# Performance work log

Measured on AMD Instinct MI355X. Metric: run time of the kernel, lower is better.

## Reference

```python
import jax, jax.numpy as jnp
import numpy as np

N_FM = 100000; N_TP = 4096; N_SM = 100000
IN_FM = 64; IN_SM = 32; IN_TP = 32; IN_GF = 64; HID = 128
E_QOQ = 1000000; E_BP = 1000000; E_CP = 500000; E_CD = 500000; E_RB = 1000000


def setup_inputs():
    key = jax.random.key(0)
    ks = jax.random.split(key, 32)
    rn = lambda k, s, sc=0.05: jax.random.normal(k, s, jnp.float32) * sc
    inp = {}
    inp['x_fm'] = jax.random.normal(ks[0], (N_FM, IN_FM), jnp.float32)
    inp['x_sm'] = jax.random.normal(ks[1], (N_SM, IN_SM), jnp.float32)
    inp['period_vol'] = jax.random.uniform(ks[2], (N_TP, 1), jnp.float32)
    inp['gf'] = jax.random.normal(ks[3], (1, IN_GF), jnp.float32)
    inp['pe_table'] = rn(ks[4], (N_TP, IN_TP), 1.0)  # period_emb weight
    inp['qoq_src'] = jax.random.randint(ks[5], (E_QOQ,), 0, N_FM)
    inp['qoq_dst'] = jax.random.randint(ks[6], (E_QOQ,), 0, N_FM)
    inp['bp_src'] = jax.random.randint(ks[7], (E_BP,), 0, N_FM)
    inp['bp_dst'] = jax.random.randint(ks[8], (E_BP,), 0, N_TP)
    inp['cp_src'] = jax.random.randint(ks[9], (E_CP,), 0, N_TP)
    inp['cp_dst'] = jax.random.randint(ks[10], (E_CP,), 0, N_FM)
    inp['cd_src'] = jax.random.randint(ks[11], (E_CD,), 0, N_TP)
    inp['cd_dst'] = jax.random.randint(ks[12], (E_CD,), 0, N_SM)
    inp['rb_src'] = jax.random.randint(ks[13], (E_RB,), 0, N_TP)
    inp['rb_dst'] = jax.random.randint(ks[14], (E_RB,), 0, N_FM)
    i = 15
    # per-relation SAGEConv params: W_l [in_src,H] + bias, W_r [in_dst,H] (root, no bias)
    for name, ins, ind in [('qoq', IN_FM, IN_FM), ('bp', IN_FM, IN_TP), ('cp', IN_TP, IN_FM), ('cd', IN_TP, IN_SM), ('rb', IN_TP, IN_FM)]:
        inp[name + '_Wl'] = rn(ks[i], (ins, HID)); inp[name + '_bl'] = jnp.zeros((HID,), jnp.float32)
        inp[name + '_Wr'] = rn(ks[i + 1], (ind, HID)); i += 2
    for t in ['fm', 'tp', 'sm']:
        inp['ln_' + t + '_g'] = jnp.ones((HID,), jnp.float32)
        inp['ln_' + t + '_b'] = jnp.zeros((HID,), jnp.float32)
    inp['head_W1'] = rn(ks[i], (HID * 3 + IN_GF, HID // 2)); inp['head_b1'] = jnp.zeros((HID // 2,), jnp.float32)
    inp['head_W2'] = rn(ks[i + 1], (HID // 2, 1)); inp['head_b2'] = jnp.zeros((1,), jnp.float32)
    return inp


def _seg_mean(feat, dst, n):
    s = jax.ops.segment_sum(feat, dst, num_segments=n)
    c = jax.ops.segment_sum(jnp.ones((dst.shape[0], 1), feat.dtype), dst, num_segments=n)
    return s / jnp.maximum(c, 1.0)


def _sage(x_src, x_dst, src, dst, Wl, bl, Wr):
    # PyG SAGEConv: lin_l(mean_j x_j) + lin_r(x_i); aggregate raw features, then transform
    m = _seg_mean(x_src[src], dst, x_dst.shape[0])
    return m @ Wl + bl + x_dst @ Wr


def _ln(x, g, b, eps=1e-5):
    mu = x.mean(-1, keepdims=True)
    xc = x - mu
    var = (xc * xc).mean(-1, keepdims=True)
    return xc / jnp.sqrt(var + eps) * g + b


def _forward(x_fm, x_sm, period_vol, gf, pe_table,
             qoq_Wl, qoq_bl, qoq_Wr, bp_Wl, bp_bl, bp_Wr, cp_Wl, cp_bl, cp_Wr,
             cd_Wl, cd_bl, cd_Wr, rb_Wl, rb_bl, rb_Wr,
             ln_fm_g, ln_fm_b, ln_tp_g, ln_tp_b, ln_sm_g, ln_sm_b,
             head_W1, head_b1, head_W2, head_b2,
             qoq_src, qoq_dst, bp_src, bp_dst, cp_src, cp_dst, cd_src, cd_dst, rb_src, rb_dst):
    pe = pe_table * period_vol  # [T, in_tp]
    # HeteroConv aggr='mean': average relation outputs per destination type
    out_fm = (_sage(x_fm, x_fm, qoq_src, qoq_dst, qoq_Wl, qoq_bl, qoq_Wr)
              + _sage(pe, x_fm, cp_src, cp_dst, cp_Wl, cp_bl, cp_Wr)
              + _sage(pe, x_fm, rb_src, rb_dst, rb_Wl, rb_bl, rb_Wr)) / 3.0
    out_tp = _sage(x_fm, pe, bp_src, bp_dst, bp_Wl, bp_bl, bp_Wr)
    out_sm = _sage(pe, x_sm, cd_src, cd_dst, cd_Wl, cd_bl, cd_Wr)
    fm = jax.nn.relu(_ln(out_fm, ln_fm_g, ln_fm_b))
    tp = jax.nn.relu(_ln(out_tp, ln_tp_g, ln_tp_b))
    sm = jax.nn.relu(_ln(out_sm, ln_sm_g, ln_sm_b))
    h = jnp.concatenate([fm.mean(0), tp.mean(0), sm.mean(0), gf[0]], axis=-1)
    h = jax.nn.relu(h @ head_W1 + head_b1)  # dropout is identity in eval
    return (h @ head_W2 + head_b2).squeeze()


def reference(x_fm, x_sm, period_vol, gf, pe_table,
              qoq_src, qoq_dst, bp_src, bp_dst, cp_src, cp_dst, cd_src, cd_dst, rb_src, rb_dst,
              qoq_Wl, qoq_bl, qoq_Wr, bp_Wl, bp_bl, bp_Wr, cp_Wl, cp_bl, cp_Wr,
              cd_Wl, cd_bl, cd_Wr, rb_Wl, rb_bl, rb_Wr,
              ln_fm_g, ln_fm_b, ln_tp_g, ln_tp_b, ln_sm_g, ln_sm_b,
              head_W1, head_b1, head_W2, head_b2):
    return _forward(x_fm, x_sm, period_vol, gf, pe_table,
                    qoq_Wl, qoq_bl, qoq_Wr, bp_Wl, bp_bl, bp_Wr, cp_Wl, cp_bl, cp_Wr,
                    cd_Wl, cd_bl, cd_Wr, rb_Wl, rb_bl, rb_Wr,
                    ln_fm_g, ln_fm_b, ln_tp_g, ln_tp_b, ln_sm_g, ln_sm_b,
                    head_W1, head_b1, head_W2, head_b2,
                    qoq_src, qoq_dst, bp_src, bp_dst, cp_src, cp_dst, cd_src, cd_dst, rb_src, rb_dst)
```

## Files before the change

### kernel.cpp

```cpp
#include <hip/hip_runtime.h>
#include <hip/hip_fp16.h>

#define N_FM 100000
#define N_TP 4096
#define N_SM 100000
#define HID 128
#define E_QOQ 1000000
#define E_BP 1000000
#define E_CP 500000
#define E_CD 500000
#define E_RB 1000000
#define E_TOT 4000000

#define EO_CP  1000000
#define EO_RB  1500000
#define EO_BP  2500000
#define EO_CD  3500000

#define EL_QOQ 0
#define EL_CP  (N_FM)
#define EL_RB  (2 * N_FM)
#define EL_BP  (3 * N_FM)
#define EL_CD  (3 * N_FM + N_TP)
#define NTOT   (3 * N_FM + N_TP + N_SM)

#define BB_QOQ 0
#define BB_CP  782
#define BB_RB  1173
#define BB_BP  1564
#define BB_CD  1692
#define NBUCK  2083
#define CHUNK  4096
#define NCHUNK ((E_TOT + CHUNK - 1) / CHUNK)
#define EPB    (CHUNK / 256)

#define PAIRS_CAP 5784064

#define GRID_FM 768
#define GRID_TP 64
#define GRID_SM 1024

__device__ __forceinline__ int bucket_base(int b) {
    if (b < BB_CP) return b * 2048;
    if (b < BB_RB) return 1601536 + (b - BB_CP) * 2048;
    if (b < BB_BP) return 2402304 + (b - BB_RB) * 3584;
    if (b < BB_CD) return 3803648 + (b - BB_BP) * 9216;
    return 4983296 + (b - BB_CD) * 2048;
}

typedef _Float16 h2 __attribute__((ext_vector_type(2)));
typedef _Float16 f16x8_t __attribute__((ext_vector_type(8)));
typedef float f32x4_t __attribute__((ext_vector_type(4)));

union U32H2 { unsigned u; h2 h; };
union U4H8 { uint4 u; f16x8_t h; };

#if defined(__has_builtin)
#if __has_builtin(__builtin_amdgcn_fdot2)
#define HAVE_FDOT2 1
#endif
#endif

__device__ __forceinline__ unsigned pk2(float a, float b) {
    U32H2 x; x.h = h2{(_Float16)a, (_Float16)b}; return x.u;
}
__device__ __forceinline__ f16x8_t as_h8(uint4 v) { U4H8 x; x.u = v; return x.h; }

__device__ __forceinline__ float dot2sel(float acc, h2 v, h2 sel) {
#ifdef HAVE_FDOT2
    return __builtin_amdgcn_fdot2(v, sel, acc, false);
#else
    return acc + (float)v[0] * (float)sel[0] + (float)v[1] * (float)sel[1];
#endif
}

#define R1 (N_FM * 32)
#define R2 (R1 + N_SM * 16)
#define R3 (R2 + N_TP * 16)
#define R4 (R3 + 12288)
#define R5 (R4 + 6144)
#define R6 (R5 + 4096)
#define R7 (R6 + 128)

__device__ __forceinline__ unsigned pack_pair(const float* W, int p, int c) {
    return pk2(W[(2 * p) * HID + c], W[(2 * p + 1) * HID + c]);
}

__global__ void pack_all(const float* __restrict__ x_fm, const float* __restrict__ x_sm,
                         const float* __restrict__ pe_table, const float* __restrict__ pvol,
                         const float* __restrict__ qoq_Wl, const float* __restrict__ cp_Wl,
                         const float* __restrict__ rb_Wl, const float* __restrict__ qoq_Wr,
                         const float* __restrict__ cp_Wr, const float* __restrict__ rb_Wr,
                         const float* __restrict__ bp_Wl, const float* __restrict__ bp_Wr,
                         const float* __restrict__ cd_Wl, const float* __restrict__ cd_Wr,
                         const float* __restrict__ qoq_bl, const float* __restrict__ cp_bl,
                         const float* __restrict__ rb_bl,
                         unsigned* __restrict__ x_fm_f, unsigned* __restrict__ x_sm_f,
                         unsigned* __restrict__ pe_f, unsigned* __restrict__ wf_fm,
                         unsigned* __restrict__ wf_tp, unsigned* __restrict__ wf_sm,
                         float* __restrict__ bias_fm) {
    int gid = blockIdx.x * blockDim.x + threadIdx.x;
    if (gid < R1) {
        float2 t = ((const float2*)x_fm)[gid];
        x_fm_f[gid] = pk2(t.x, t.y);
    } else if (gid < R2) {
        int i = gid - R1;
        float2 t = ((const float2*)x_sm)[i];
        x_sm_f[i] = pk2(t.x, t.y);
    } else if (gid < R3) {
        int i = gid - R2;
        float2 t = ((const float2*)pe_table)[i];
        float v = pvol[i >> 4];
        pe_f[i] = pk2(t.x * v, t.y * v);
    } else if (gid < R4) {
        int j = gid - R3;
        int f = j >> 8, lr = (j >> 2) & 63, jj = j & 3;
        int p = (f >> 3) * 16 + ((lr >> 4) << 2) + jj;
        int c = (f & 7) * 16 + (lr & 15);
        unsigned v;
        if (p < 32) v = pack_pair(qoq_Wl, p, c);
        else if (p < 48) v = pack_pair(cp_Wl, p - 32, c);
        else if (p < 64) v = pack_pair(rb_Wl, p - 48, c);
        else {
            int pp = p - 64;
            float u0 = qoq_Wr[(2 * pp) * HID + c] + cp_Wr[(2 * pp) * HID + c] + rb_Wr[(2 * pp) * HID + c];
            float u1 = qoq_Wr[(2 * pp + 1) * HID + c] + cp_Wr[(2 * pp + 1) * HID + c] + rb_Wr[(2 * pp + 1) * HID + c];
            v = pk2(u0, u1);
        }
        wf_fm[j] = v;
    } else if (gid < R5) {
        int j = gid - R4;
        int f = j >> 8, lr = (j >> 2) & 63, jj = j & 3;
        int p = (f >> 3) * 16 + ((lr >> 4) << 2) + jj;
        int c = (f & 7) * 16 + (lr & 15);
        wf_tp[j] = (p < 32) ? pack_pair(bp_Wl, p, c) : pack_pair(bp_Wr, p - 32, c);
    } else if (gid < R6) {
        int j = gid - R5;
        int f = j >> 8, lr = (j >> 2) & 63, jj = j & 3;
        int p = (f >> 3) * 16 + ((lr >> 4) << 2) + jj;
        int c = (f & 7) * 16 + (lr & 15);
        wf_sm[j] = (p < 16) ? pack_pair(cd_Wl, p, c) : pack_pair(cd_Wr, p - 16, c);
    } else if (gid < R7) {
        int c = gid - R6;
        bias_fm[c] = qoq_bl[c] + cp_bl[c] + rb_bl[c];
    }
}

struct EdgePtrs {
    const int *qs, *qd, *cs, *cd_, *rs, *rd, *bs, *bd, *ds, *dd;
};

template <bool NEED_SRC>
__device__ __forceinline__ void edge_decode(const EdgePtrs& P, int e, int& bucket, int& dl, int& src) {
    const int* dp = P.qd; const int* sp = P.qs;
    int i = e, bb = BB_QOQ, sh = 7;
    if (e >= EO_CP) { i = e - EO_CP; dp = P.cd_; sp = P.cs; bb = BB_CP; sh = 8; }
    if (e >= EO_RB) { i = e - EO_RB; dp = P.rd;  sp = P.rs; bb = BB_RB; sh = 8; }
    if (e >= EO_BP) { i = e - EO_BP; dp = P.bd;  sp = P.bs; bb = BB_BP; sh = 5; }
    if (e >= EO_CD) { i = e - EO_CD; dp = P.dd;  sp = P.ds; bb = BB_CD; sh = 8; }
    int d = dp[i];
    bucket = bb + (d >> sh);
    dl = d & ((1 << sh) - 1);
    if (NEED_SRC) src = sp[i];
}

__global__ void __launch_bounds__(256) bin_kernel(EdgePtrs P, int* __restrict__ bwork,
                                                  unsigned* __restrict__ pairs) {
    __shared__ int lh[NBUCK];
    const int tid = threadIdx.x;
    for (int i = tid; i < NBUCK; i += 256) lh[i] = 0;
    __syncthreads();
    const int base = blockIdx.x * CHUNK;
    const int lim = min(base + CHUNK, E_TOT);
    unsigned ebd[EPB]; int esr[EPB];
#pragma unroll
    for (int j = 0; j < EPB; j++) {
        int e = base + tid + j * 256;
        if (e < lim) {
            int b, dl, s;
            edge_decode<true>(P, e, b, dl, s);
            ebd[j] = ((unsigned)b << 8) | (unsigned)dl;
            esr[j] = s;
            atomicAdd(&lh[b], 1);
        }
    }
    __syncthreads();
#pragma unroll
    for (int u = 0; u < (NBUCK + 255) / 256; u++) {
        int b = tid + u * 256;
        if (b < NBUCK) {
            int c = lh[b];
            lh[b] = c ? bucket_base(b) + atomicAdd(&bwork[b], c) : 0;
        }
    }
    __syncthreads();
#pragma unroll
    for (int j = 0; j < EPB; j++) {
        int e = base + tid + j * 256;
        if (e < lim) {
            int b = (int)(ebd[j] >> 8);
            int pos = atomicAdd(&lh[b], 1);
            pairs[pos] = ((ebd[j] & 255u) << 24) | (unsigned)esr[j];
        }
    }
}

__global__ void __launch_bounds__(256) esort(const int* __restrict__ bwork,
                                             const unsigned* __restrict__ pairs,
                                             int* __restrict__ so,
                                             int* __restrict__ el_beg, int* __restrict__ el_end) {
    __shared__ int hist[256], scn[256];
    __shared__ int so_lds[9216];
    const int b = blockIdx.x;
    const int tid = threadIdx.x;
    int beg = bucket_base(b);
    int end = beg + bwork[b];
    int egbase, ne;
    if (b < BB_CP)      { int e0 = (b - BB_QOQ) << 7; egbase = EL_QOQ + e0; ne = min(128, N_FM - e0); }
    else if (b < BB_RB) { int e0 = (b - BB_CP) << 8;  egbase = EL_CP + e0;  ne = min(256, N_FM - e0); }
    else if (b < BB_BP) { int e0 = (b - BB_RB) << 8;  egbase = EL_RB + e0;  ne = min(256, N_FM - e0); }
    else if (b < BB_CD) { int e0 = (b - BB_BP) << 5;  egbase = EL_BP + e0;  ne = min(32, N_TP - e0); }
    else                { int e0 = (b - BB_CD) << 8;  egbase = EL_CD + e0;  ne = min(256, N_SM - e0); }
    hist[tid] = 0;
    __syncthreads();
    for (int e = beg + tid; e < end; e += 256)
        atomicAdd(&hist[pairs[e] >> 24], 1);
    __syncthreads();
    int v = hist[tid];
    scn[tid] = v;
    __syncthreads();
    for (int off = 1; off < 256; off <<= 1) {
        int u = (tid >= off) ? scn[tid - off] : 0;
        __syncthreads();
        scn[tid] += u;
        __syncthreads();
    }
    int excl = scn[tid] - v;
    if (tid < ne) {
        el_beg[egbase + tid] = beg + excl;
        el_end[egbase + tid] = beg + excl + v;
    }
    hist[tid] = excl;
    __syncthreads();
    for (int e = beg + tid; e < end; e += 256) {
        unsigned pr = pairs[e];
        int dl = pr >> 24;
        int pos = atomicAdd(&hist[dl], 1);
        so_lds[pos] = (int)(pr & 0xFFFFFF);
    }
    __syncthreads();
    const int n = end - beg;
    for (int i = tid; i < n; i += 256) so[beg + i] = so_lds[i];
}

template <int LOGP>
__device__ __forceinline__ void gather_one(int g, int lane, const int* __restrict__ begs,
                                           const int* __restrict__ ends,
                                           const int* __restrict__ ssrc,
                                           const unsigned* __restrict__ feat,
                                           unsigned* __restrict__ mean) {
    const int P = 1 << LOGP;
    const h2 SLO = h2{(_Float16)1.0f, (_Float16)0.0f};
    const h2 SHI = h2{(_Float16)0.0f, (_Float16)1.0f};
    int beg = begs[g], end = ends[g];
    float alo = 0.0f, ahi = 0.0f;
    int i = beg;
    for (; i + 8 <= end; i += 8) {
        int s0 = ssrc[i],     s1 = ssrc[i + 1], s2 = ssrc[i + 2], s3 = ssrc[i + 3];
        int s4 = ssrc[i + 4], s5 = ssrc[i + 5], s6 = ssrc[i + 6], s7 = ssrc[i + 7];
        unsigned v0 = feat[(size_t)s0 * P + lane];
        unsigned v1 = feat[(size_t)s1 * P + lane];
        unsigned v2 = feat[(size_t)s2 * P + lane];
        unsigned v3 = feat[(size_t)s3 * P + lane];
        unsigned v4 = feat[(size_t)s4 * P + lane];
        unsigned v5 = feat[(size_t)s5 * P + lane];
        unsigned v6 = feat[(size_t)s6 * P + lane];
        unsigned v7 = feat[(size_t)s7 * P + lane];
        U32H2 u;
        u.u = v0; alo = dot2sel(alo, u.h, SLO); ahi = dot2sel(ahi, u.h, SHI);
        u.u = v1; alo = dot2sel(alo, u.h, SLO); ahi = dot2sel(ahi, u.h, SHI);
        u.u = v2; alo = dot2sel(alo, u.h, SLO); ahi = dot2sel(ahi, u.h, SHI);
        u.u = v3; alo = dot2sel(alo, u.h, SLO); ahi = dot2sel(ahi, u.h, SHI);
        u.u = v4; alo = dot2sel(alo, u.h, SLO); ahi = dot2sel(ahi, u.h, SHI);
        u.u = v5; alo = dot2sel(alo, u.h, SLO); ahi = dot2sel(ahi, u.h, SHI);
        u.u = v6; alo = dot2sel(alo, u.h, SLO); ahi = dot2sel(ahi, u.h, SHI);
        u.u = v7; alo = dot2sel(alo, u.h, SLO); ahi = dot2sel(ahi, u.h, SHI);
    }
    for (; i + 2 <= end; i += 2) {
        int s0 = ssrc[i], s1 = ssrc[i + 1];
        unsigned v0 = feat[(size_t)s0 * P + lane];
        unsigned v1 = feat[(size_t)s1 * P + lane];
        U32H2 u;
        u.u = v0; alo = dot2sel(alo, u.h, SLO); ahi = dot2sel(ahi, u.h, SHI);
        u.u = v1; alo = dot2sel(alo, u.h, SLO); ahi = dot2sel(ahi, u.h, SHI);
    }
    if (i < end) {
        unsigned v = feat[(size_t)ssrc[i] * P + lane];
        U32H2 u; u.u = v;
        alo = dot2sel(alo, u.h, SLO); ahi = dot2sel(ahi, u.h, SHI);
    }
    float ic = (end > beg) ? 1.0f / (float)(end - beg) : 0.0f;
    mean[(size_t)g * P + lane] = pk2(alo * ic, ahi * ic);
}

#define G1 (N_TP * 32)
#define G2 (G1 + N_FM * 32)
#define G3 (G2 + N_FM * 16)
#define G4 (G3 + N_SM * 16)
#define G5 (G4 + N_FM * 16)

__global__ void gather_all(const int* __restrict__ el_beg, const int* __restrict__ el_end,
                           const int* __restrict__ so_all,
                           const unsigned* __restrict__ x_fm_f, const unsigned* __restrict__ pe_f,
                           unsigned* __restrict__ mean_qoq, unsigned* __restrict__ mean_cp,
                           unsigned* __restrict__ mean_rb, unsigned* __restrict__ mean_bp,
                           unsigned* __restrict__ mean_cd) {
    int gid = blockIdx.x * blockDim.x + threadIdx.x;
    if (gid < G1) {
        gather_one<5>(gid >> 5, gid & 31, el_beg + EL_BP, el_end + EL_BP, so_all, x_fm_f, mean_bp);
    } else if (gid < G2) {
        int i = gid - G1;
        gather_one<5>(i >> 5, i & 31, el_beg + EL_QOQ, el_end + EL_QOQ, so_all, x_fm_f, mean_qoq);
    } else if (gid < G3) {
        int i = gid - G2;
        gather_one<4>(i >> 4, i & 15, el_beg + EL_CP, el_end + EL_CP, so_all, pe_f, mean_cp);
    } else if (gid < G4) {
        int i = gid - G3;
        gather_one<4>(i >> 4, i & 15, el_beg + EL_CD, el_end + EL_CD, so_all, pe_f, mean_cd);
    } else if (gid < G5) {
        int i = gid - G4;
        gather_one<4>(i >> 4, i & 15, el_beg + EL_RB, el_end + EL_RB, so_all, pe_f, mean_rb);
    }
}


__global__ void __launch_bounds__(256)
fm_mfma(const unsigned* __restrict__ mq, const unsigned* __restrict__ mc,
        const unsigned* __restrict__ mr, const unsigned* __restrict__ xf,
        const unsigned* __restrict__ wfrag, const float* __restrict__ bias,
        const float* __restrict__ ln_g, const float* __restrict__ ln_b,
        float* __restrict__ part) {
    __shared__ uint4 wlds[48 * 64];
    const int tid = threadIdx.x, lane = tid & 63, wid = tid >> 6;
    for (int i = tid; i < 48 * 64; i += 256) wlds[i] = ((const uint4*)wfrag)[i];
    const int c0 = lane & 15, ko = lane >> 4;
    float bias_[8], g_[8], b_[8], colacc[8];
#pragma unroll
    for (int nt = 0; nt < 8; nt++) {
        int c = nt * 16 + c0;
        bias_[nt] = bias[c]; g_[nt] = ln_g[c]; b_[nt] = ln_b[c]; colacc[nt] = 0.0f;
    }
    __syncthreads();
    const f32x4_t zero = {0.0f, 0.0f, 0.0f, 0.0f};
    const int ntiles = N_FM / 16;
    for (int tile = blockIdx.x * 4 + wid; tile < ntiles; tile += gridDim.x * 4) {
        const size_t row = (size_t)tile * 16 + c0;
        uint4 av[6];
        av[0] = ((const uint4*)mq)[row * 8 + ko];
        av[1] = ((const uint4*)mq)[row * 8 + 4 + ko];
        av[2] = ((const uint4*)mc)[row * 4 + ko];
        av[3] = ((const uint4*)mr)[row * 4 + ko];
        av[4] = ((const uint4*)xf)[row * 8 + ko];
        av[5] = ((const uint4*)xf)[row * 8 + 4 + ko];
        f32x4_t acc[8];
#pragma unroll
        for (int nt = 0; nt < 8; nt++) acc[nt] = zero;
#pragma unroll
        for (int ks = 0; ks < 6; ks++) {
            f16x8_t af = as_h8(av[ks]);
#pragma unroll
            for (int nt = 0; nt < 8; nt++)
                acc[nt] = __builtin_amdgcn_mfma_f32_16x16x32_f16(
                    af, as_h8(wlds[(ks * 8 + nt) * 64 + lane]), acc[nt], 0, 0, 0);
        }
#pragma unroll
        for (int r = 0; r < 4; r++) {
            float yv[8]; float s = 0.0f, q = 0.0f;
#pragma unroll
            for (int nt = 0; nt < 8; nt++) {
                float y = (acc[nt][r] + bias_[nt]) * (1.0f / 3.0f);
                yv[nt] = y; s += y; q += y * y;
            }
#pragma unroll
            for (int off = 1; off < 16; off <<= 1) { s += __shfl_xor(s, off); q += __shfl_xor(q, off); }
            float mu = s * (1.0f / 128.0f);
            float var = fmaxf(q * (1.0f / 128.0f) - mu * mu, 0.0f);
            float rs = rsqrtf(var + 1e-5f);
#pragma unroll
            for (int nt = 0; nt < 8; nt++)
                colacc[nt] += fmaxf((yv[nt] - mu) * rs * g_[nt] + b_[nt], 0.0f);
        }
    }
#pragma unroll
    for (int nt = 0; nt < 8; nt++) {
        colacc[nt] += __shfl_xor(colacc[nt], 16);
        colacc[nt] += __shfl_xor(colacc[nt], 32);
    }
    __syncthreads();
    float* sred = (float*)wlds;
    if (lane < 16) {
#pragma unroll
        for (int nt = 0; nt < 8; nt++) sred[wid * 128 + nt * 16 + lane] = colacc[nt];
    }
    __syncthreads();
    if (tid < 128)
        part[(size_t)blockIdx.x * 128 + tid] =
            sred[tid] + sred[128 + tid] + sred[256 + tid] + sred[384 + tid];
}

template <int KSA, int KSB>
__global__ void __launch_bounds__(256)
rows_mfma(int ntiles, const unsigned* __restrict__ mA, const unsigned* __restrict__ xB,
          const unsigned* __restrict__ wfrag, const float* __restrict__ bl,
          const float* __restrict__ ln_g, const float* __restrict__ ln_b,
          float* __restrict__ part) {
    constexpr int KS = KSA + KSB;
    __shared__ uint4 wlds[KS * 8 * 64];
    const int tid = threadIdx.x, lane = tid & 63, wid = tid >> 6;
    for (int i = tid; i < KS * 8 * 64; i += 256) wlds[i] = ((const uint4*)wfrag)[i];
    const int c0 = lane & 15, ko = lane >> 4;
    float bias_[8], g_[8], b_[8], colacc[8];
#pragma unroll
    for (int nt = 0; nt < 8; nt++) {
        int c = nt * 16 + c0;
        bias_[nt] = bl[c]; g_[nt] = ln_g[c]; b_[nt] = ln_b[c]; colacc[nt] = 0.0f;
    }
    __syncthreads();
    const f32x4_t zero = {0.0f, 0.0f, 0.0f, 0.0f};
    for (int tile = blockIdx.x * 4 + wid; tile < ntiles; tile += gridDim.x * 4) {
        const size_t row = (size_t)tile * 16 + c0;
        uint4 av[KS];
#pragma unroll
        for (int ks = 0; ks < KSA; ks++) av[ks] = ((const uint4*)mA)[row * (KSA * 4) + ks * 4 + ko];
#pragma unroll
        for (int ks = 0; ks < KSB; ks++) av[KSA + ks] = ((const uint4*)xB)[row * (KSB * 4) + ks * 4 + ko];
        f32x4_t acc[8];
#pragma unroll
        for (int nt = 0; nt < 8; nt++) acc[nt] = zero;
#pragma unroll
        for (int ks = 0; ks < KS; ks++) {
            f16x8_t af = as_h8(av[ks]);
#pragma unroll
            for (int nt = 0; nt < 8; nt++)
                acc[nt] = __builtin_amdgcn_mfma_f32_16x16x32_f16(
                    af, as_h8(wlds[(ks * 8 + nt) * 64 + lane]), acc[nt], 0, 0, 0);
        }
#pragma unroll
        for (int r = 0; r < 4; r++) {
            float yv[8]; float s = 0.0f, q = 0.0f;
#pragma unroll
            for (int nt = 0; nt < 8; nt++) {
                float y = acc[nt][r] + bias_[nt];
                yv[nt] = y; s += y; q += y * y;
            }
#pragma unroll
            for (int off = 1; off < 16; off <<= 1) { s += __shfl_xor(s, off); q += __shfl_xor(q, off); }
            float mu = s * (1.0f / 128.0f);
            float var = fmaxf(q * (1.0f / 128.0f) - mu * mu, 0.0f);
            float rs = rsqrtf(var + 1e-5f);
#pragma unroll
            for (int nt = 0; nt < 8; nt++)
                colacc[nt] += fmaxf((yv[nt] - mu) * rs * g_[nt] + b_[nt], 0.0f);
        }
    }
#pragma unroll
    for (int nt = 0; nt < 8; nt++) {
        colacc[nt] += __shfl_xor(colacc[nt], 16);
        colacc[nt] += __shfl_xor(colacc[nt], 32);
    }
    __syncthreads();
    float* sred = (float*)wlds;
    if (lane < 16) {
#pragma unroll
        for (int nt = 0; nt < 8; nt++) sred[wid * 128 + nt * 16 + lane] = colacc[nt];
    }
    __syncthreads();
    if (tid < 128)
        part[(size_t)blockIdx.x * 128 + tid] =
            sred[tid] + sred[128 + tid] + sred[256 + tid] + sred[384 + tid];
}

__global__ void __launch_bounds__(512)
reduce_cols(const float* __restrict__ part, float* __restrict__ colsum) {
    __shared__ float lds[512];
    const int t = threadIdx.x, col = t & 127, sl = t >> 7;
    int cnt, srcoff, dst;
    if (blockIdx.x == 0)      { cnt = GRID_FM; srcoff = 0;                         dst = 0;   }
    else if (blockIdx.x == 1) { cnt = GRID_TP; srcoff = GRID_FM * 128;             dst = 128; }
    else                      { cnt = GRID_SM; srcoff = (GRID_FM + GRID_TP) * 128; dst = 256; }
    float a = 0.0f;
    for (int i = sl; i < cnt; i += 4) a += part[srcoff + i * 128 + col];
    lds[t] = a;
    __syncthreads();
    if (t < 128) colsum[dst + t] = lds[t] + lds[128 + t] + lds[256 + t] + lds[384 + t];
}

__global__ void head_kernel(const float* __restrict__ colsum, const float* __restrict__ gf,
                            const float* __restrict__ W1, const float* __restrict__ b1,
                            const float* __restrict__ W2, const float* __restrict__ b2,
                            float* __restrict__ out) {
    __shared__ float h[448];
    __shared__ float sh[512];
    __shared__ float h1[64];
    int t = threadIdx.x;
    if (t < 128) h[t] = colsum[t] * (1.0f / N_FM);
    else if (t < 256) h[t] = colsum[t] * (1.0f / N_TP);
    else if (t < 384) h[t] = colsum[t] * (1.0f / N_SM);
    else if (t < 448) h[t] = gf[t - 384];
    __syncthreads();
    {
        int col = t & 63, slice = t >> 6;
        float a = 0.0f;
        for (int k = slice * 56; k < slice * 56 + 56; k++) a += h[k] * W1[k * 64 + col];
        sh[slice * 64 + col] = a;
    }
    __syncthreads();
    if (t < 64) {
        float a = b1[t];
#pragma unroll
        for (int s = 0; s < 8; s++) a += sh[s * 64 + t];
        h1[t] = fmaxf(a, 0.0f);
    }
    __syncthreads();
    if (t < 64) {
        float p = h1[t] * W2[t];
#pragma unroll
        for (int off = 1; off < 64; off <<= 1) p += __shfl_xor(p, off);
        if (t == 0) out[0] = p + b2[0];
    }
}

extern "C" void kernel_launch(void* const* d_in, const int* in_sizes, int n_in,
                              void* d_out, int out_size, void* d_ws, size_t ws_size,
                              hipStream_t stream) {
    const float* x_fm = (const float*)d_in[0];
    const float* x_sm = (const float*)d_in[1];
    const float* period_vol = (const float*)d_in[2];
    const float* gf = (const float*)d_in[3];
    const float* pe_table = (const float*)d_in[4];
    const int* qoq_src = (const int*)d_in[5];
    const int* qoq_dst = (const int*)d_in[6];
    const int* bp_src = (const int*)d_in[7];
    const int* bp_dst = (const int*)d_in[8];
    const int* cp_src = (const int*)d_in[9];
    const int* cp_dst = (const int*)d_in[10];
    const int* cd_src = (const int*)d_in[11];
    const int* cd_dst = (const int*)d_in[12];
    const int* rb_src = (const int*)d_in[13];
    const int* rb_dst = (const int*)d_in[14];
    const float* qoq_Wl = (const float*)d_in[15];
    const float* qoq_bl = (const float*)d_in[16];
    const float* qoq_Wr = (const float*)d_in[17];
    const float* bp_Wl = (const float*)d_in[18];
    const float* bp_bl = (const float*)d_in[19];
    const float* bp_Wr = (const float*)d_in[20];
    const float* cp_Wl = (const float*)d_in[21];
    const float* cp_bl = (const float*)d_in[22];
    const float* cp_Wr = (const float*)d_in[23];
    const float* cd_Wl = (const float*)d_in[24];
    const float* cd_bl = (const float*)d_in[25];
    const float* cd_Wr = (const float*)d_in[26];
    const float* rb_Wl = (const float*)d_in[27];
    const float* rb_bl = (const float*)d_in[28];
    const float* rb_Wr = (const float*)d_in[29];
    const float* ln_fm_g = (const float*)d_in[30];
    const float* ln_fm_b = (const float*)d_in[31];
    const float* ln_tp_g = (const float*)d_in[32];
    const float* ln_tp_b = (const float*)d_in[33];
    const float* ln_sm_g = (const float*)d_in[34];
    const float* ln_sm_b = (const float*)d_in[35];
    const float* head_W1 = (const float*)d_in[36];
    const float* head_b1 = (const float*)d_in[37];
    const float* head_W2 = (const float*)d_in[38];
    const float* head_b2 = (const float*)d_in[39];

    unsigned* wsu = (unsigned*)d_ws;
    size_t off = 0;
    int* bwork = (int*)(wsu + off); off += NBUCK;
    float* colsum = (float*)(wsu + off); off += 384;
    size_t zero_words = off;
    off = (off + 3) & ~(size_t)3;
    unsigned* pairs = wsu + off; off += PAIRS_CAP;
    int* so_all = (int*)(wsu + off); off += PAIRS_CAP;
    int* el_beg = (int*)(wsu + off); off += NTOT;
    int* el_end = (int*)(wsu + off); off += NTOT;
    unsigned* mean_qoq = wsu + off; off += (size_t)N_FM * 32;
    unsigned* mean_cp  = wsu + off; off += (size_t)N_FM * 16;
    unsigned* mean_rb  = wsu + off; off += (size_t)N_FM * 16;
    unsigned* mean_bp  = wsu + off; off += (size_t)N_TP * 32;
    unsigned* mean_cd  = wsu + off; off += (size_t)N_SM * 16;
    unsigned* pe_f     = wsu + off; off += (size_t)N_TP * 16;
    unsigned* x_fm_f   = wsu + off; off += (size_t)N_FM * 32;
    unsigned* x_sm_f   = wsu + off; off += (size_t)N_SM * 16;
    unsigned* wf_fm    = wsu + off; off += 12288;
    unsigned* wf_tp    = wsu + off; off += 6144;
    unsigned* wf_sm    = wsu + off; off += 4096;
    float* bias_fm     = (float*)(wsu + off); off += 128;

    float* part_fm = (float*)pairs;
    float* part_tp = part_fm + GRID_FM * 128;
    float* part_sm = part_tp + GRID_TP * 128;

    hipMemsetAsync(d_ws, 0, zero_words * 4, stream);

    pack_all<<<(R7 + 255) / 256, 256, 0, stream>>>(
        x_fm, x_sm, pe_table, period_vol, qoq_Wl, cp_Wl, rb_Wl, qoq_Wr, cp_Wr, rb_Wr,
        bp_Wl, bp_Wr, cd_Wl, cd_Wr, qoq_bl, cp_bl, rb_bl,
        x_fm_f, x_sm_f, pe_f, wf_fm, wf_tp, wf_sm, bias_fm);

    EdgePtrs EP{qoq_src, qoq_dst, cp_src, cp_dst, rb_src, rb_dst, bp_src, bp_dst, cd_src, cd_dst};

    bin_kernel<<<NCHUNK, 256, 0, stream>>>(EP, bwork, pairs);
    esort<<<NBUCK, 256, 0, stream>>>(bwork, pairs, so_all, el_beg, el_end);
    gather_all<<<(G5 + 255) / 256, 256, 0, stream>>>(el_beg, el_end, so_all, x_fm_f, pe_f,
                                                     mean_qoq, mean_cp, mean_rb, mean_bp, mean_cd);

    fm_mfma<<<GRID_FM, 256, 0, stream>>>(mean_qoq, mean_cp, mean_rb, x_fm_f, wf_fm,
                                         bias_fm, ln_fm_g, ln_fm_b, part_fm);
    rows_mfma<2, 1><<<GRID_TP, 256, 0, stream>>>(N_TP / 16, mean_bp, pe_f, wf_tp,
                                                 bp_bl, ln_tp_g, ln_tp_b, part_tp);
    rows_mfma<1, 1><<<GRID_SM, 256, 0, stream>>>(N_SM / 16, mean_cd, x_sm_f, wf_sm,
                                                 cd_bl, ln_sm_g, ln_sm_b, part_sm);

    reduce_cols<<<3, 512, 0, stream>>>(part_fm, colsum);

    head_kernel<<<1, 512, 0, stream>>>(colsum, gf, head_W1, head_b1, head_W2, head_b2,
                                       (float*)d_out);
}
```

Baseline: 439.4 us.

## Restructure gather: block-per-TP node and two-nodes-per-wave edge splitting

Replaces the one-thread-group-per-destination gather with a new work split. Each of the 4096 high-degree bp destinations now gets a full 256-thread block that splits its edge list across 8 sub-groups and combines them through shared memory. The other relations assign two destinations per wavefront, spreading each destination's edges across sub-lanes and reducing with cross-lane shuffles. The intent is to balance load and expose more memory-level parallelism for bp's long edge lists. The cost is predicated loads, extra reductions, and reliance on el_end of node gA equalling el_beg of node gA+1, which holds only if edge lists are contiguous.

```diff
diff --git a/kernel.cpp b/kernel.cpp
--- a/kernel.cpp
+++ b/kernel.cpp
@@ -39,6 +39,10 @@
 #define GRID_FM 768
 #define GRID_TP 64
 #define GRID_SM 1024
+
+#define GW_REL 50000
+#define GB_REL (GW_REL / 4)
+#define GATHER_GRID (N_TP + 4 * GB_REL)
 
 __device__ __forceinline__ int bucket_base(int b) {
     if (b < BB_CP) return b * 2048;
@@ -254,82 +258,106 @@
 }
 
 template <int LOGP>
-__device__ __forceinline__ void gather_one(int g, int lane, const int* __restrict__ begs,
-                                           const int* __restrict__ ends,
-                                           const int* __restrict__ ssrc,
-                                           const unsigned* __restrict__ feat,
-                                           unsigned* __restrict__ mean) {
-    const int P = 1 << LOGP;
+__device__ __forceinline__ void gather_wave2(int gA, const int* __restrict__ eb,
+                                             const int* __restrict__ ee,
+                                             const int* __restrict__ ssrc,
+                                             const unsigned* __restrict__ feat,
+                                             unsigned* __restrict__ mean, int lane) {
+    const int P = 1 << LOGP, STR = 64 >> LOGP;
     const h2 SLO = h2{(_Float16)1.0f, (_Float16)0.0f};
     const h2 SHI = h2{(_Float16)0.0f, (_Float16)1.0f};
-    int beg = begs[g], end = ends[g];
-    float alo = 0.0f, ahi = 0.0f;
-    int i = beg;
-    for (; i + 8 <= end; i += 8) {
-        int s0 = ssrc[i],     s1 = ssrc[i + 1], s2 = ssrc[i + 2], s3 = ssrc[i + 3];
-        int s4 = ssrc[i + 4], s5 = ssrc[i + 5], s6 = ssrc[i + 6], s7 = ssrc[i + 7];
-        unsigned v0 = feat[(size_t)s0 * P + lane];
-        unsigned v1 = feat[(size_t)s1 * P + lane];
-        unsigned v2 = feat[(size_t)s2 * P + lane];
-        unsigned v3 = feat[(size_t)s3 * P + lane];
-        unsigned v4 = feat[(size_t)s4 * P + lane];
-        unsigned v5 = feat[(size_t)s5 * P + lane];
-        unsigned v6 = feat[(size_t)s6 * P + lane];
-        unsigned v7 = feat[(size_t)s7 * P + lane];
-        U32H2 u;
-        u.u = v0; alo = dot2sel(alo, u.h, SLO); ahi = dot2sel(ahi, u.h, SHI);
-        u.u = v1; alo = dot2sel(alo, u.h, SLO); ahi = dot2sel(ahi, u.h, SHI);
-        u.u = v2; alo = dot2sel(alo, u.h, SLO); ahi = dot2sel(ahi, u.h, SHI);
-        u.u = v3; alo = dot2sel(alo, u.h, SLO); ahi = dot2sel(ahi, u.h, SHI);
-        u.u = v4; alo = dot2sel(alo, u.h, SLO); ahi = dot2sel(ahi, u.h, SHI);
-        u.u = v5; alo = dot2sel(alo, u.h, SLO); ahi = dot2sel(ahi, u.h, SHI);
-        u.u = v6; alo = dot2sel(alo, u.h, SLO); ahi = dot2sel(ahi, u.h, SHI);
-        u.u = v7; alo = dot2sel(alo, u.h, SLO); ahi = dot2sel(ahi, u.h, SHI);
-    }
-    for (; i + 2 <= end; i += 2) {
-        int s0 = ssrc[i], s1 = ssrc[i + 1];
-        unsigned v0 = feat[(size_t)s0 * P + lane];
-        unsigned v1 = feat[(size_t)s1 * P + lane];
-        U32H2 u;
-        u.u = v0; alo = dot2sel(alo, u.h, SLO); ahi = dot2sel(ahi, u.h, SHI);
-        u.u = v1; alo = dot2sel(alo, u.h, SLO); ahi = dot2sel(ahi, u.h, SHI);
-    }
-    if (i < end) {
-        unsigned v = feat[(size_t)ssrc[i] * P + lane];
-        U32H2 u; u.u = v;
-        alo = dot2sel(alo, u.h, SLO); ahi = dot2sel(ahi, u.h, SHI);
-    }
-    float ic = (end > beg) ? 1.0f / (float)(end - beg) : 0.0f;
-    mean[(size_t)g * P + lane] = pk2(alo * ic, ahi * ic);
-}
-
-#define G1 (N_TP * 32)
-#define G2 (G1 + N_FM * 32)
-#define G3 (G2 + N_FM * 16)
-#define G4 (G3 + N_SM * 16)
-#define G5 (G4 + N_FM * 16)
-
-__global__ void gather_all(const int* __restrict__ el_beg, const int* __restrict__ el_end,
-                           const int* __restrict__ so_all,
-                           const unsigned* __restrict__ x_fm_f, const unsigned* __restrict__ pe_f,
-                           unsigned* __restrict__ mean_qoq, unsigned* __restrict__ mean_cp,
-                           unsigned* __restrict__ mean_rb, unsigned* __restrict__ mean_bp,
-                           unsigned* __restrict__ mean_cd) {
-    int gid = blockIdx.x * blockDim.x + threadIdx.x;
-    if (gid < G1) {
-        gather_one<5>(gid >> 5, gid & 31, el_beg + EL_BP, el_end + EL_BP, so_all, x_fm_f, mean_bp);
-    } else if (gid < G2) {
-        int i = gid - G1;
-        gather_one<5>(i >> 5, i & 31, el_beg + EL_QOQ, el_end + EL_QOQ, so_all, x_fm_f, mean_qoq);
-    } else if (gid < G3) {
-        int i = gid - G2;
-        gather_one<4>(i >> 4, i & 15, el_beg + EL_CP, el_end + EL_CP, so_all, pe_f, mean_cp);
-    } else if (gid < G4) {
-        int i = gid - G3;
-        gather_one<4>(i >> 4, i & 15, el_beg + EL_CD, el_end + EL_CD, so_all, pe_f, mean_cd);
-    } else if (gid < G5) {
-        int i = gid - G4;
-        gather_one<4>(i >> 4, i & 15, el_beg + EL_RB, el_end + EL_RB, so_all, pe_f, mean_rb);
+    int begA = eb[gA];
+    int begB = eb[gA + 1];
+    int endA = begB;
+    int endB = ee[gA + 1];
+    const int sub = lane >> LOGP, fl = lane & (P - 1);
+    float aloA = 0.0f, ahiA = 0.0f, aloB = 0.0f, ahiB = 0.0f;
+    for (int base = 0; begA + base < endA || begB + base < endB; base += 8 * STR) {
+        int sA[8], sB[8];
+#pragma unroll
+        for (int j = 0; j < 8; j++) {
+            int ia = begA + base + j * STR + sub;
+            int ib = begB + base + j * STR + sub;
+            sA[j] = (ia < endA) ? ssrc[ia] : -1;
+            sB[j] = (ib < endB) ? ssrc[ib] : -1;
+        }
+#pragma unroll
+        for (int j = 0; j < 8; j++) {
+            if (sA[j] >= 0) {
+                U32H2 u; u.u = feat[(unsigned)sA[j] * P + fl];
+                aloA = dot2sel(aloA, u.h, SLO); ahiA = dot2sel(ahiA, u.h, SHI);
+            }
+            if (sB[j] >= 0) {
+                U32H2 u; u.u = feat[(unsigned)sB[j] * P + fl];
+                aloB = dot2sel(aloB, u.h, SLO); ahiB = dot2sel(ahiB, u.h, SHI);
+            }
+        }
+    }
+#pragma unroll
+    for (int off = P; off < 64; off <<= 1) {
+        aloA += __shfl_xor(aloA, off); ahiA += __shfl_xor(ahiA, off);
+        aloB += __shfl_xor(aloB, off); ahiB += __shfl_xor(ahiB, off);
+    }
+    if (lane < P) {
+        float icA = (endA > begA) ? 1.0f / (float)(endA - begA) : 0.0f;
+        float icB = (endB > begB) ? 1.0f / (float)(endB - begB) : 0.0f;
+        mean[(size_t)gA * P + lane] = pk2(aloA * icA, ahiA * icA);
+        mean[((size_t)gA + 1) * P + lane] = pk2(aloB * icB, ahiB * icB);
+    }
+}
+
+__global__ void __launch_bounds__(256)
+gather_all(const int* __restrict__ el_beg, const int* __restrict__ el_end,
+           const int* __restrict__ so_all,
+           const unsigned* __restrict__ x_fm_f, const unsigned* __restrict__ pe_f,
+           unsigned* __restrict__ mean_qoq, unsigned* __restrict__ mean_cp,
+           unsigned* __restrict__ mean_rb, unsigned* __restrict__ mean_bp,
+           unsigned* __restrict__ mean_cd) {
+    __shared__ float red[8][64];
+    const int blk = blockIdx.x, tid = threadIdx.x;
+    if (blk < N_TP) {
+        const h2 SLO = h2{(_Float16)1.0f, (_Float16)0.0f};
+        const h2 SHI = h2{(_Float16)0.0f, (_Float16)1.0f};
+        const int g = blk;
+        const int beg = el_beg[EL_BP + g], end = el_end[EL_BP + g];
+        const int sub = tid >> 5, fl = tid & 31;
+        float alo = 0.0f, ahi = 0.0f;
+        for (int base = 0; beg + base < end; base += 64) {
+            int s[8];
+#pragma unroll
+            for (int j = 0; j < 8; j++) {
+                int idx = beg + base + j * 8 + sub;
+                s[j] = (idx < end) ? so_all[idx] : -1;
+            }
+#pragma unroll
+            for (int j = 0; j < 8; j++) {
+                if (s[j] >= 0) {
+                    U32H2 u; u.u = x_fm_f[(unsigned)s[j] * 32 + fl];
+                    alo = dot2sel(alo, u.h, SLO); ahi = dot2sel(ahi, u.h, SHI);
+                }
+            }
+        }
+        red[sub][fl] = alo; red[sub][fl + 32] = ahi;
+        __syncthreads();
+        if (tid < 32) {
+            float a = 0.0f, h = 0.0f;
+#pragma unroll
+            for (int k = 0; k < 8; k++) { a += red[k][tid]; h += red[k][tid + 32]; }
+            float ic = (end > beg) ? 1.0f / (float)(end - beg) : 0.0f;
+            mean_bp[(size_t)g * 32 + tid] = pk2(a * ic, h * ic);
+        }
+        return;
+    }
+    const int w = (blk - N_TP) * 4 + (tid >> 6);
+    const int lane = tid & 63;
+    if (w < GW_REL) {
+        gather_wave2<5>(2 * w, el_beg + EL_QOQ, el_end + EL_QOQ, so_all, x_fm_f, mean_qoq, lane);
+    } else if (w < 2 * GW_REL) {
+        gather_wave2<4>(2 * (w - GW_REL), el_beg + EL_CP, el_end + EL_CP, so_all, pe_f, mean_cp, lane);
+    } else if (w < 3 * GW_REL) {
+        gather_wave2<4>(2 * (w - 2 * GW_REL), el_beg + EL_CD, el_end + EL_CD, so_all, pe_f, mean_cd, lane);
+    } else {
+        gather_wave2<4>(2 * (w - 3 * GW_REL), el_beg + EL_RB, el_end + EL_RB, so_all, pe_f, mean_rb, lane);
     }
 }
 
@@ -612,8 +640,8 @@
 
     bin_kernel<<<NCHUNK, 256, 0, stream>>>(EP, bwork, pairs);
     esort<<<NBUCK, 256, 0, stream>>>(bwork, pairs, so_all, el_beg, el_end);
-    gather_all<<<(G5 + 255) / 256, 256, 0, stream>>>(el_beg, el_end, so_all, x_fm_f, pe_f,
-                                                     mean_qoq, mean_cp, mean_rb, mean_bp, mean_cd);
+    gather_all<<<GATHER_GRID, 256, 0, stream>>>(el_beg, el_end, so_all, x_fm_f, pe_f,
+                                                mean_qoq, mean_cp, mean_rb, mean_bp, mean_cd);
 
     fm_mfma<<<GRID_FM, 256, 0, stream>>>(mean_qoq, mean_cp, mean_rb, x_fm_f, wf_fm,
                                          bias_fm, ln_fm_g, ln_fm_b, part_fm);
```

Measured after the change: 477.7 us. 1.09x slower.
